# Performance work log

Measured on AMD Instinct MI355X. Metric: run time of the kernel, lower is better.

## Reference

```python
import jax, jax.numpy as jnp
import numpy as np

B, S, V, E, HID = 16, 40, 1004, 256, 256
C, R, HW = 1024, 256, 32  # featureChannel, releMapChannel, spatial
BN_EPS = 1e-5


def setup_inputs() -> dict:
    key = jax.random.key(0)
    ks = jax.random.split(key, 16)
    sc = 0.05
    emb = jax.random.normal(ks[4], (V, E), jnp.float32) * sc
    emb = emb.at[0].set(0.0)  # padding_idx = 0
    return {
        "feature": jax.random.normal(ks[0], (B, C, HW, HW), jnp.float32),
        "depth": jax.random.uniform(ks[1], (B, 1, HW, HW), jnp.float32),
        "instruction_idx": jax.random.randint(ks[2], (B, S), 0, V, jnp.int32),
        "instruction_length": jnp.clip(jax.random.randint(ks[3], (B,), 1, S + 1, jnp.int32), 1, S),
        "only_train_rele": 1,
        "emb_table": emb,
        "w_ih": jax.random.normal(ks[5], (4 * HID, E), jnp.float32) * sc,
        "w_hh": jax.random.normal(ks[6], (4 * HID, HID), jnp.float32) * sc,
        "b_ih": jax.random.normal(ks[7], (4 * HID,), jnp.float32) * sc,
        "b_hh": jax.random.normal(ks[8], (4 * HID,), jnp.float32) * sc,
        "e2d_w": jax.random.normal(ks[9], (HID, HID), jnp.float32) * sc,
        "e2d_b": jax.random.normal(ks[10], (HID,), jnp.float32) * sc,
        "lin1_w": jax.random.normal(ks[11], (R * C, HID), jnp.float32) * sc,
        "lin1_b": jax.random.normal(ks[12], (R * C,), jnp.float32) * sc,
        "bn_gamma": jnp.ones((R,), jnp.float32),
        "bn_beta": jnp.zeros((R,), jnp.float32),
        "bn_mean": jax.random.normal(ks[13], (R,), jnp.float32) * 0.01,
        "bn_var": jnp.ones((R,), jnp.float32),
    }


def _encoder_lstm(idx, lengths, emb_table, w_ih, w_hh, b_ih, b_hh, e2d_w, e2d_b):
    # Faithful to packed-sequence LSTM: state stops updating at each sample's length.
    embeds = emb_table[idx]                      # [B,S,E]
    xs = jnp.swapaxes(embeds, 0, 1)              # [S,B,E]
    mask = (jnp.arange(S)[:, None] < lengths[None, :])  # [S,B]
    h0 = jnp.zeros((B, HID), embeds.dtype)
    c0 = jnp.zeros((B, HID), embeds.dtype)

    def step(carry, xm):
        h, c = carry
        x_t, m = xm                              # [B,E], [B]
        gates = x_t @ w_ih.T + h @ w_hh.T + (b_ih + b_hh)  # [B,4H]
        i, f, g, o = jnp.split(gates, 4, axis=-1)  # torch gate order: i,f,g,o
        c_new = jax.nn.sigmoid(f) * c + jax.nn.sigmoid(i) * jnp.tanh(g)
        h_new = jax.nn.sigmoid(o) * jnp.tanh(c_new)
        m = m[:, None]
        return (jnp.where(m, h_new, h), jnp.where(m, c_new, c)), None

    (h_t, _), _ = jax.lax.scan(step, (h0, c0), (xs, mask))
    return jnp.tanh(h_t @ e2d_w.T + e2d_b)       # [B,HID]


def reference(feature, depth, instruction_idx, instruction_length, only_train_rele,
              emb_table, w_ih, w_hh, b_ih, b_hh, e2d_w, e2d_b,
              lin1_w, lin1_b, bn_gamma, bn_beta, bn_mean, bn_var):
    instr = _encoder_lstm(instruction_idx, instruction_length, emb_table,
                          w_ih, w_hh, b_ih, b_hh, e2d_w, e2d_b)  # [B,HID]
    # per-sample dynamic 1x1 filters (dropout in eval mode -> identity)
    f1 = jax.nn.leaky_relu(instr @ lin1_w.T + lin1_b, negative_slope=0.01)
    f1 = f1.reshape(B, R, C)
    # batched per-sample 1x1 conv: one einsum replaces the batch loop of F.conv2d
    rele = jax.nn.relu(jnp.einsum('bchw,brc->brhw', feature, f1))  # [B,R,H,W]
    # BatchNorm2d in eval mode with running stats
    scale = bn_gamma / jnp.sqrt(bn_var + BN_EPS)
    rele = rele * scale[None, :, None, None] + (bn_beta - bn_mean * scale)[None, :, None, None]
    single = jnp.max(rele, axis=1)               # channel-max pooling -> [B,H,W]
    return jnp.clip(single, 0.0, 1.0)
```

## Files before the change

### kernel.cpp

```cpp
#include <hip/hip_runtime.h>
#include <hip/hip_fp16.h>
#include <math.h>

#define NB 16
#define SQ 40
#define HIDN 256
#define CC 1024
#define NROW 262144

#define AGENT __HIP_MEMORY_SCOPE_AGENT
#define SENT 0x7E7E7E7Eu

__device__ __forceinline__ float sigf(float x){ return 1.0f/(1.0f+__expf(-x)); }

typedef _Float16 h2v __attribute__((ext_vector_type(2)));
typedef _Float16 f16x8 __attribute__((ext_vector_type(8)));
typedef float    f32x4 __attribute__((ext_vector_type(4)));

__device__ __forceinline__ float fd2(unsigned w, unsigned h, float acc){
  h2v a = __builtin_bit_cast(h2v, w);
  h2v b = __builtin_bit_cast(h2v, h);
#if __has_builtin(__builtin_amdgcn_fdot2)
  return __builtin_amdgcn_fdot2(a, b, acc, false);
#else
  return acc + (float)a.x*(float)b.x + (float)a.y*(float)b.y;
#endif
}

__device__ __forceinline__ unsigned pkh(float lo, float hi){
  return (unsigned)__half_as_ushort(__float2half_rn(lo))
       | ((unsigned)__half_as_ushort(__float2half_rn(hi)) << 16);
}

__global__ __launch_bounds__(256) void k_xgates(
    const int* __restrict__ idx, const float* __restrict__ emb,
    const float* __restrict__ w_ih, const float* __restrict__ b_ih,
    const float* __restrict__ b_hh, float* __restrict__ XG)
{
  __shared__ float xs[8*256];
  int t = threadIdx.x;
  int tb0 = blockIdx.x * 8;
  #pragma unroll
  for (int i = 0; i < 8; ++i) {
    int flat = t + i*256;
    int p = flat >> 8, k = flat & 255;
    int tb = tb0 + p;
    int ts = tb >> 4, b = tb & 15;
    int row = idx[b*SQ + ts];
    xs[p*256 + k] = emb[row*256 + k];
  }
  __syncthreads();
  int rows[4];
  float acc[4][8];
  #pragma unroll
  for (int r = 0; r < 4; ++r) {
    rows[r] = t + r*256;
    float bias = b_ih[rows[r]] + b_hh[rows[r]];
    #pragma unroll
    for (int p = 0; p < 8; ++p) acc[r][p] = bias;
  }
  for (int k16 = 0; k16 < 16; ++k16) {
    float4 w[4][4];
    #pragma unroll
    for (int r = 0; r < 4; ++r)
      #pragma unroll
      for (int q = 0; q < 4; ++q)
        w[r][q] = *(const float4*)&w_ih[rows[r]*256 + k16*16 + q*4];
    #pragma unroll
    for (int p = 0; p < 8; ++p) {
      #pragma unroll
      for (int q = 0; q < 4; ++q) {
        float4 x = *(const float4*)&xs[p*256 + k16*16 + q*4];
        #pragma unroll
        for (int r = 0; r < 4; ++r)
          acc[r][p] += w[r][q].x*x.x + w[r][q].y*x.y + w[r][q].z*x.z + w[r][q].w*x.w;
      }
    }
  }
  #pragma unroll
  for (int p = 0; p < 8; ++p)
    #pragma unroll
    for (int r = 0; r < 4; ++r)
      XG[(tb0 + p)*1024 + rows[r]] = acc[r][p];
}

__global__ __launch_bounds__(256) void k_whh3(const float* __restrict__ w, unsigned* __restrict__ W3)
{
  int tid = blockIdx.x*256 + threadIdx.x;
  int c    = tid & 3;
  int tt   = (tid >> 2) & 511;
  int q    = (tid >> 11) & 31;
  int half = tid >> 16;
  int pair = 4*q + c;
  int g = tt >> 7, j = tt & 127;
  int row = g*256 + half*128 + j;
  float2 v = *(const float2*)&w[(size_t)row*256 + 2*pair];
  W3[tid] = pkh(v.x, v.y);
}

__global__ __launch_bounds__(512) void k_lstm2(
    const float* __restrict__ XG, const uint4* __restrict__ W3,
    const int* __restrict__ lens, const float* __restrict__ e2d_w,
    const float* __restrict__ e2d_b, float* __restrict__ instr,
    unsigned* __restrict__ hcomm)
{
  __shared__ float dot_s[512];
  __shared__ float h_s[128];
  __shared__ float h_e[256];

  int t = threadIdx.x;
  int b    = blockIdx.x & 15;
  int half = blockIdx.x >> 4;
  int len  = lens[b];
  int lane = t & 63;

  unsigned wv[128];
  {
    const uint4* wp = W3 + (size_t)half*32*512 + t;
    #pragma unroll
    for (int q = 0; q < 32; ++q) {
      uint4 v = wp[(size_t)q*512];
      wv[4*q+0]=v.x; wv[4*q+1]=v.y; wv[4*q+2]=v.z; wv[4*q+3]=v.w;
    }
  }

  int g = t >> 7, j = t & 127;
  int row = g*256 + half*128 + j;
  float c_reg = 0.0f, h_reg = 0.0f;

  for (int it = 0; it < SQ; ++it) {
    float acc = XG[(it*NB + b)*1024 + row];
    if (it > 0) {
      unsigned own = pkh(h_s[2*lane], h_s[2*lane + 1]);
      int owni = (int)own;
      const unsigned* oslot = hcomm + ((it-1)*NB + b)*128 + (half ? 0 : 64);
      if (half == 0) {
        #pragma unroll
        for (int q = 0; q < 64; ++q)
          acc = fd2(wv[q], (unsigned)__builtin_amdgcn_readlane(owni, q), acc);
        unsigned oth;
        do { oth = __hip_atomic_load(oslot + lane, __ATOMIC_RELAXED, AGENT); }
        while (__any((int)(oth == SENT)));
        int othi = (int)oth;
        #pragma unroll
        for (int q = 0; q < 64; ++q)
          acc = fd2(wv[64+q], (unsigned)__builtin_amdgcn_readlane(othi, q), acc);
      } else {
        #pragma unroll
        for (int q = 0; q < 64; ++q)
          acc = fd2(wv[64+q], (unsigned)__builtin_amdgcn_readlane(owni, q), acc);
        unsigned oth;
        do { oth = __hip_atomic_load(oslot + lane, __ATOMIC_RELAXED, AGENT); }
        while (__any((int)(oth == SENT)));
        int othi = (int)oth;
        #pragma unroll
        for (int q = 0; q < 64; ++q)
          acc = fd2(wv[q], (unsigned)__builtin_amdgcn_readlane(othi, q), acc);
      }
    }
    dot_s[t] = acc;
    __syncthreads();
    if (t < 128) {
      float iv = sigf (dot_s[t]);
      float fv = sigf (dot_s[t + 128]);
      float gv = tanhf(dot_s[t + 256]);
      float ov = sigf (dot_s[t + 384]);
      float cn = fv*c_reg + iv*gv;
      float hn = ov*tanhf(cn);
      if (it < len) { c_reg = cn; h_reg = hn; }
      h_s[t] = h_reg;
    }
    __syncthreads();
    if (t < 64)
      __hip_atomic_store(hcomm + (it*NB + b)*128 + half*64 + t,
                         pkh(h_s[2*t], h_s[2*t+1]), __ATOMIC_RELAXED, AGENT);
  }

  if (half == 0) {
    const unsigned* slot = hcomm + ((SQ-1)*NB + b)*128;
    if (t < 64) {
      unsigned v0, v1;
      do {
        v0 = __hip_atomic_load(slot + t,      __ATOMIC_RELAXED, AGENT);
        v1 = __hip_atomic_load(slot + 64 + t, __ATOMIC_RELAXED, AGENT);
      } while (__any((int)(v0 == SENT)) || __any((int)(v1 == SENT)));
      h2v lo = __builtin_bit_cast(h2v, v0);
      h2v hi = __builtin_bit_cast(h2v, v1);
      h_e[2*t]       = (float)lo.x;  h_e[2*t + 1]       = (float)lo.y;
      h_e[128 + 2*t] = (float)hi.x;  h_e[128 + 2*t + 1] = (float)hi.y;
    }
    __syncthreads();
    if (t < 256) {
      float acc2 = e2d_b[t];
      const float4* wp2 = (const float4*)&e2d_w[t*256];
      #pragma unroll 8
      for (int k4 = 0; k4 < 64; ++k4) {
        float4 w = wp2[k4];
        float4 h4 = *(const float4*)&h_e[k4*4];
        acc2 += w.x*h4.x + w.y*h4.y + w.z*h4.z + w.w*h4.w;
      }
      instr[b*256 + t] = tanhf(acc2);
    }
  }
}

__global__ __launch_bounds__(256) void k_lin1(
    const float* __restrict__ instr, const float* __restrict__ w,
    const float* __restrict__ bias, _Float16* __restrict__ f1h)
{
  __shared__ float is[4096];
  int t = threadIdx.x;
  #pragma unroll
  for (int i = 0; i < 16; ++i) is[t + i*256] = instr[t + i*256];
  __syncthreads();
  int r0 = blockIdx.x*512 + t;
  int r1 = r0 + 256;
  const float* w0 = &w[(size_t)r0*256];
  const float* w1 = &w[(size_t)r1*256];
  float acc0[16], acc1[16];
  float bz0 = bias[r0], bz1 = bias[r1];
  #pragma unroll
  for (int i = 0; i < 16; ++i){ acc0[i]=bz0; acc1[i]=bz1; }
  for (int k16 = 0; k16 < 16; ++k16) {
    float4 a[4], bb[4];
    #pragma unroll
    for (int q = 0; q < 4; ++q){
      a[q]  = *(const float4*)&w0[k16*16 + q*4];
      bb[q] = *(const float4*)&w1[k16*16 + q*4];
    }
    #pragma unroll
    for (int bi = 0; bi < 16; ++bi) {
      #pragma unroll
      for (int q = 0; q < 4; ++q) {
        float4 x = *(const float4*)&is[bi*256 + k16*16 + q*4];
        acc0[bi] += a[q].x*x.x + a[q].y*x.y + a[q].z*x.z + a[q].w*x.w;
        acc1[bi] += bb[q].x*x.x + bb[q].y*x.y + bb[q].z*x.z + bb[q].w*x.w;
      }
    }
  }
  #pragma unroll
  for (int bi = 0; bi < 16; ++bi) {
    float v0 = acc0[bi]; v0 = v0 > 0.0f ? v0 : 0.01f*v0;
    float v1 = acc1[bi]; v1 = v1 > 0.0f ? v1 : 0.01f*v1;
    f1h[(size_t)bi*NROW + r0] = (_Float16)v0;
    f1h[(size_t)bi*NROW + r1] = (_Float16)v1;
  }
}

__global__ __launch_bounds__(256, 1) void k_einsum_mfma(
    const uint4* __restrict__ f1h4, const float* __restrict__ feat,
    const float* __restrict__ gamma, const float* __restrict__ beta,
    const float* __restrict__ mean, const float* __restrict__ var,
    float* __restrict__ out)
{
  __shared__ unsigned ALDS[256*20];
  __shared__ unsigned BLDS[128*20];
  __shared__ float sc_s[256], sh_s[256];
  __shared__ float red[2][128];

  int t = threadIdx.x;
  int b  = blockIdx.x >> 3;
  int P0 = (blockIdx.x & 7) * 128;
  int wid  = t >> 6, lane = t & 63;
  int wp = wid & 1, wr = wid >> 1;
  int col = lane & 15, quad = lane >> 4;

  {
    float s = gamma[t] * rsqrtf(var[t] + 1e-5f);
    sc_s[t] = s;
    sh_s[t] = beta[t] - mean[t]*s;
  }

  f32x4 acc[8][4];
  #pragma unroll
  for (int mt = 0; mt < 8; ++mt)
    #pragma unroll
    for (int nt = 0; nt < 4; ++nt) acc[mt][nt] = (f32x4)0.0f;

  const uint4* arow = f1h4 + ((size_t)b*NROW + (size_t)t*1024)/8;
  int p_loc = t & 127, khalf = t >> 7;
  const float* bbase = feat + ((size_t)b*1024 + khalf*16)*1024 + P0 + p_loc;

  uint4 apf[4];
  float bpf[16];
  #pragma unroll
  for (int g = 0; g < 4; ++g) apf[g] = arow[g];
  #pragma unroll
  for (int j = 0; j < 16; ++j) bpf[j] = bbase[(size_t)j*1024];

  for (int kc = 0; kc < 32; ++kc) {
    __syncthreads();
    #pragma unroll
    for (int g = 0; g < 4; ++g)
      *(uint4*)&ALDS[t*20 + g*4] = apf[g];
    {
      unsigned u[8];
      #pragma unroll
      for (int i = 0; i < 8; ++i) u[i] = pkh(bpf[2*i], bpf[2*i+1]);
      uint4 w0 = {u[0],u[1],u[2],u[3]}, w1 = {u[4],u[5],u[6],u[7]};
      *(uint4*)&BLDS[p_loc*20 + khalf*8]     = w0;
      *(uint4*)&BLDS[p_loc*20 + khalf*8 + 4] = w1;
    }
    __syncthreads();
    if (kc + 1 < 32) {
      #pragma unroll
      for (int g = 0; g < 4; ++g) apf[g] = arow[(kc+1)*4 + g];
      const float* bb = bbase + (size_t)(kc+1)*32*1024;
      #pragma unroll
      for (int j = 0; j < 16; ++j) bpf[j] = bb[(size_t)j*1024];
    }
    f16x8 bf[4];
    #pragma unroll
    for (int nt = 0; nt < 4; ++nt) {
      uint4 raw = *(const uint4*)&BLDS[(wp*64 + nt*16 + col)*20 + quad*4];
      bf[nt] = __builtin_bit_cast(f16x8, raw);
    }
    #pragma unroll
    for (int mt = 0; mt < 8; ++mt) {
      uint4 raw = *(const uint4*)&ALDS[(wr*128 + mt*16 + col)*20 + quad*4];
      f16x8 af = __builtin_bit_cast(f16x8, raw);
      #pragma unroll
      for (int nt = 0; nt < 4; ++nt)
        acc[mt][nt] = __builtin_amdgcn_mfma_f32_16x16x32_f16(af, bf[nt], acc[mt][nt], 0, 0, 0);
    }
  }

  float pmax[4];
  #pragma unroll
  for (int nt = 0; nt < 4; ++nt) pmax[nt] = -3.4e38f;
  #pragma unroll
  for (int mt = 0; mt < 8; ++mt) {
    int rb = wr*128 + mt*16 + quad*4;
    f32x4 scv = *(const f32x4*)&sc_s[rb];
    f32x4 shv = *(const f32x4*)&sh_s[rb];
    #pragma unroll
    for (int nt = 0; nt < 4; ++nt) {
      f32x4 a = acc[mt][nt];
      #pragma unroll
      for (int reg = 0; reg < 4; ++reg) {
        float v = fmaxf(a[reg], 0.0f)*scv[reg] + shv[reg];
        pmax[nt] = fmaxf(pmax[nt], v);
      }
    }
  }
  #pragma unroll
  for (int nt = 0; nt < 4; ++nt) {
    float m = pmax[nt];
    m = fmaxf(m, __shfl_xor(m, 16));
    m = fmaxf(m, __shfl_xor(m, 32));
    if (lane < 16) red[wr][wp*64 + nt*16 + lane] = m;
  }
  __syncthreads();
  if (t < 128) {
    float v = fmaxf(red[0][t], red[1][t]);
    out[b*1024 + P0 + t] = fminf(fmaxf(v, 0.0f), 1.0f);
  }
}

extern "C" void kernel_launch(void* const* d_in, const int* in_sizes, int n_in,
                              void* d_out, int out_size, void* d_ws, size_t ws_size,
                              hipStream_t stream)
{
  const float* feature = (const float*)d_in[0];
  const int*   idx     = (const int*)d_in[2];
  const int*   lens    = (const int*)d_in[3];
  const float* emb     = (const float*)d_in[5];
  const float* w_ih    = (const float*)d_in[6];
  const float* w_hh    = (const float*)d_in[7];
  const float* b_ih    = (const float*)d_in[8];
  const float* b_hh    = (const float*)d_in[9];
  const float* e2d_w   = (const float*)d_in[10];
  const float* e2d_b   = (const float*)d_in[11];
  const float* lin1_w  = (const float*)d_in[12];
  const float* lin1_b  = (const float*)d_in[13];
  const float* gamma   = (const float*)d_in[14];
  const float* beta    = (const float*)d_in[15];
  const float* mean    = (const float*)d_in[16];
  const float* var     = (const float*)d_in[17];

  char* ws = (char*)d_ws;
  float*    XG     = (float*)(ws);
  float*    instr  = (float*)(ws + 2621440);
  unsigned* W3     = (unsigned*)(ws + 2637824);
  unsigned* hcomm  = (unsigned*)(ws + 3162112);
  _Float16* f1h    = (_Float16*)(ws + 3489792);

  hipMemsetAsync(hcomm, 0x7E, 327680, stream);
  k_xgates <<<80,  256, 0, stream>>>(idx, emb, w_ih, b_ih, b_hh, XG);
  k_whh3   <<<512, 256, 0, stream>>>(w_hh, W3);
  k_lstm2  <<<32,  512, 0, stream>>>(XG, (const uint4*)W3, lens, e2d_w, e2d_b, instr, hcomm);
  k_lin1   <<<512, 256, 0, stream>>>(instr, lin1_w, lin1_b, f1h);
  k_einsum_mfma <<<128, 256, 0, stream>>>((const uint4*)f1h, feature, gamma, beta, mean, var,
                                          (float*)d_out);
}
```

Baseline: 614.7 us.

## Double grid size for lin1 and einsum kernels, prefetch LSTM input gates

k_lin1 now computes one output row per thread instead of two and launches twice as many blocks. k_einsum_mfma shrinks each block's pixel tile from 128 to 64, regrids the B-tile loading and the warp-to-row mapping, and launches 256 blocks so more of the CUs on the device are busy. The LSTM loop also prefetches the next step's XG value so its load latency can overlap the recurrent dot product. The trade-off is that the shared instr and f1 tiles are re-read by more blocks, adding redundant global traffic.

Measured after the change: 601.0 us. -2.2%, faster.

```diff
diff --git a/kernel.cpp b/kernel.cpp
--- a/kernel.cpp
+++ b/kernel.cpp
@@ -128,8 +128,11 @@
   int row = g*256 + half*128 + j;
   float c_reg = 0.0f, h_reg = 0.0f;
 
+  float xg_cur = XG[(0*NB + b)*1024 + row];
+
   for (int it = 0; it < SQ; ++it) {
-    float acc = XG[(it*NB + b)*1024 + row];
+    float xg_next = (it+1 < SQ) ? XG[((it+1)*NB + b)*1024 + row] : 0.0f;
+    float acc = xg_cur;
     if (it > 0) {
       unsigned own = pkh(h_s[2*lane], h_s[2*lane + 1]);
       int owni = (int)own;
@@ -174,6 +177,7 @@
     if (t < 64)
       __hip_atomic_store(hcomm + (it*NB + b)*128 + half*64 + t,
                          pkh(h_s[2*t], h_s[2*t+1]), __ATOMIC_RELAXED, AGENT);
+    xg_cur = xg_next;
   }
 
   if (half == 0) {
@@ -213,37 +217,30 @@
   #pragma unroll
   for (int i = 0; i < 16; ++i) is[t + i*256] = instr[t + i*256];
   __syncthreads();
-  int r0 = blockIdx.x*512 + t;
-  int r1 = r0 + 256;
+  int r0 = blockIdx.x*256 + t;
   const float* w0 = &w[(size_t)r0*256];
-  const float* w1 = &w[(size_t)r1*256];
-  float acc0[16], acc1[16];
-  float bz0 = bias[r0], bz1 = bias[r1];
-  #pragma unroll
-  for (int i = 0; i < 16; ++i){ acc0[i]=bz0; acc1[i]=bz1; }
+  float acc0[16];
+  float bz0 = bias[r0];
+  #pragma unroll
+  for (int i = 0; i < 16; ++i) acc0[i] = bz0;
   for (int k16 = 0; k16 < 16; ++k16) {
-    float4 a[4], bb[4];
-    #pragma unroll
-    for (int q = 0; q < 4; ++q){
-      a[q]  = *(const float4*)&w0[k16*16 + q*4];
-      bb[q] = *(const float4*)&w1[k16*16 + q*4];
-    }
+    float4 a[4];
+    #pragma unroll
+    for (int q = 0; q < 4; ++q)
+      a[q] = *(const float4*)&w0[k16*16 + q*4];
     #pragma unroll
     for (int bi = 0; bi < 16; ++bi) {
       #pragma unroll
       for (int q = 0; q < 4; ++q) {
         float4 x = *(const float4*)&is[bi*256 + k16*16 + q*4];
         acc0[bi] += a[q].x*x.x + a[q].y*x.y + a[q].z*x.z + a[q].w*x.w;
-        acc1[bi] += bb[q].x*x.x + bb[q].y*x.y + bb[q].z*x.z + bb[q].w*x.w;
       }
     }
   }
   #pragma unroll
   for (int bi = 0; bi < 16; ++bi) {
     float v0 = acc0[bi]; v0 = v0 > 0.0f ? v0 : 0.01f*v0;
-    float v1 = acc1[bi]; v1 = v1 > 0.0f ? v1 : 0.01f*v1;
     f1h[(size_t)bi*NROW + r0] = (_Float16)v0;
-    f1h[(size_t)bi*NROW + r1] = (_Float16)v1;
   }
 }
 
@@ -254,15 +251,14 @@
     float* __restrict__ out)
 {
   __shared__ unsigned ALDS[256*20];
-  __shared__ unsigned BLDS[128*20];
+  __shared__ unsigned BLDS[64*20];
   __shared__ float sc_s[256], sh_s[256];
-  __shared__ float red[2][128];
+  __shared__ float red[4][64];
 
   int t = threadIdx.x;
-  int b  = blockIdx.x >> 3;
-  int P0 = (blockIdx.x & 7) * 128;
-  int wid  = t >> 6, lane = t & 63;
-  int wp = wid & 1, wr = wid >> 1;
+  int b  = blockIdx.x >> 4;
+  int P0 = (blockIdx.x & 15) * 64;
+  int wr = t >> 6, lane = t & 63;
   int col = lane & 15, quad = lane >> 4;
 
   {
@@ -271,22 +267,22 @@
     sh_s[t] = beta[t] - mean[t]*s;
   }
 
-  f32x4 acc[8][4];
-  #pragma unroll
-  for (int mt = 0; mt < 8; ++mt)
+  f32x4 acc[4][4];
+  #pragma unroll
+  for (int mt = 0; mt < 4; ++mt)
     #pragma unroll
     for (int nt = 0; nt < 4; ++nt) acc[mt][nt] = (f32x4)0.0f;
 
   const uint4* arow = f1h4 + ((size_t)b*NROW + (size_t)t*1024)/8;
-  int p_loc = t & 127, khalf = t >> 7;
-  const float* bbase = feat + ((size_t)b*1024 + khalf*16)*1024 + P0 + p_loc;
+  int p_loc = t & 63, kq = t >> 6;
+  const float* bbase = feat + ((size_t)b*1024 + kq*8)*1024 + P0 + p_loc;
 
   uint4 apf[4];
-  float bpf[16];
+  float bpf[8];
   #pragma unroll
   for (int g = 0; g < 4; ++g) apf[g] = arow[g];
   #pragma unroll
-  for (int j = 0; j < 16; ++j) bpf[j] = bbase[(size_t)j*1024];
+  for (int j = 0; j < 8; ++j) bpf[j] = bbase[(size_t)j*1024];
 
   for (int kc = 0; kc < 32; ++kc) {
     __syncthreads();
@@ -294,12 +290,11 @@
     for (int g = 0; g < 4; ++g)
       *(uint4*)&ALDS[t*20 + g*4] = apf[g];
     {
-      unsigned u[8];
-      #pragma unroll
-      for (int i = 0; i < 8; ++i) u[i] = pkh(bpf[2*i], bpf[2*i+1]);
-      uint4 w0 = {u[0],u[1],u[2],u[3]}, w1 = {u[4],u[5],u[6],u[7]};
-      *(uint4*)&BLDS[p_loc*20 + khalf*8]     = w0;
-      *(uint4*)&BLDS[p_loc*20 + khalf*8 + 4] = w1;
+      unsigned u[4];
+      #pragma unroll
+      for (int c = 0; c < 4; ++c) u[c] = pkh(bpf[2*c], bpf[2*c+1]);
+      uint4 w0 = {u[0],u[1],u[2],u[3]};
+      *(uint4*)&BLDS[p_loc*20 + kq*4] = w0;
     }
     __syncthreads();
     if (kc + 1 < 32) {
@@ -307,17 +302,17 @@
       for (int g = 0; g < 4; ++g) apf[g] = arow[(kc+1)*4 + g];
       const float* bb = bbase + (size_t)(kc+1)*32*1024;
       #pragma unroll
-      for (int j = 0; j < 16; ++j) bpf[j] = bb[(size_t)j*1024];
+      for (int j = 0; j < 8; ++j) bpf[j] = bb[(size_t)j*1024];
     }
     f16x8 bf[4];
     #pragma unroll
     for (int nt = 0; nt < 4; ++nt) {
-      uint4 raw = *(const uint4*)&BLDS[(wp*64 + nt*16 + col)*20 + quad*4];
+      uint4 raw = *(const uint4*)&BLDS[(nt*16 + col)*20 + quad*4];
       bf[nt] = __builtin_bit_cast(f16x8, raw);
     }
     #pragma unroll
-    for (int mt = 0; mt < 8; ++mt) {
-      uint4 raw = *(const uint4*)&ALDS[(wr*128 + mt*16 + col)*20 + quad*4];
+    for (int mt = 0; mt < 4; ++mt) {
+      uint4 raw = *(const uint4*)&ALDS[(wr*64 + mt*16 + col)*20 + quad*4];
       f16x8 af = __builtin_bit_cast(f16x8, raw);
       #pragma unroll
       for (int nt = 0; nt < 4; ++nt)
@@ -329,8 +324,8 @@
   #pragma unroll
   for (int nt = 0; nt < 4; ++nt) pmax[nt] = -3.4e38f;
   #pragma unroll
-  for (int mt = 0; mt < 8; ++mt) {
-    int rb = wr*128 + mt*16 + quad*4;
+  for (int mt = 0; mt < 4; ++mt) {
+    int rb = wr*64 + mt*16 + quad*4;
     f32x4 scv = *(const f32x4*)&sc_s[rb];
     f32x4 shv = *(const f32x4*)&sh_s[rb];
     #pragma unroll
@@ -348,11 +343,11 @@
     float m = pmax[nt];
     m = fmaxf(m, __shfl_xor(m, 16));
     m = fmaxf(m, __shfl_xor(m, 32));
-    if (lane < 16) red[wr][wp*64 + nt*16 + lane] = m;
+    if (lane < 16) red[wr][nt*16 + lane] = m;
   }
   __syncthreads();
-  if (t < 128) {
-    float v = fmaxf(red[0][t], red[1][t]);
+  if (t < 64) {
+    float v = fmaxf(fmaxf(red[0][t], red[1][t]), fmaxf(red[2][t], red[3][t]));
     out[b*1024 + P0 + t] = fminf(fmaxf(v, 0.0f), 1.0f);
   }
 }
@@ -386,10 +381,10 @@
   _Float16* f1h    = (_Float16*)(ws + 3489792);
 
   hipMemsetAsync(hcomm, 0x7E, 327680, stream);
-  k_xgates <<<80,  256, 0, stream>>>(idx, emb, w_ih, b_ih, b_hh, XG);
-  k_whh3   <<<512, 256, 0, stream>>>(w_hh, W3);
-  k_lstm2  <<<32,  512, 0, stream>>>(XG, (const uint4*)W3, lens, e2d_w, e2d_b, instr, hcomm);
-  k_lin1   <<<512, 256, 0, stream>>>(instr, lin1_w, lin1_b, f1h);
-  k_einsum_mfma <<<128, 256, 0, stream>>>((const uint4*)f1h, feature, gamma, beta, mean, var,
+  k_xgates <<<80,   256, 0, stream>>>(idx, emb, w_ih, b_ih, b_hh, XG);
+  k_whh3   <<<512,  256, 0, stream>>>(w_hh, W3);
+  k_lstm2  <<<32,   512, 0, stream>>>(XG, (const uint4*)W3, lens, e2d_w, e2d_b, instr, hcomm);
+  k_lin1   <<<1024, 256, 0, stream>>>(instr, lin1_w, lin1_b, f1h);
+  k_einsum_mfma <<<256, 256, 0, stream>>>((const uint4*)f1h, feature, gamma, beta, mean, var,
                                           (float*)d_out);
 }
```
